# Kernel tuning notes

Measured on AMD Instinct MI355X. Metric: run time of the kernel, lower is better.

Reference implementation:

```python
import jax, jax.numpy as jnp
import numpy as np
from jax import lax

HID = 512   # hidden_dim
DI = 1024   # d_inner = ssm_ratio * hidden_dim
N = 64      # ssm_d_state
R = 32      # dt_rank = ceil(512/16)
K = 4       # k_group
B, H, W = 4, 32, 32
MLP = 2048  # mlp_ratio * hidden_dim


def _ln(x, w, b):
    m = x.mean(-1, keepdims=True)
    v = ((x - m) ** 2).mean(-1, keepdims=True)
    return (x - m) / jnp.sqrt(v + 1e-5) * w + b


def setup_inputs() -> dict:
    key = jax.random.key(0)
    ks = jax.random.split(key, 12)
    rn = lambda k, s, sc: jax.random.normal(k, s, jnp.float32) * sc
    inp = {}
    inp["content"] = rn(ks[0], (B, H, W, HID), 1.0)
    inp["style"] = rn(ks[1], (B, H, W, HID), 1.0)
    inp["norm1_w"] = jnp.ones((HID,), jnp.float32)
    inp["norm1_b"] = jnp.zeros((HID,), jnp.float32)
    inp["in_proj_w"] = rn(ks[2], (HID, 2 * DI), HID ** -0.5)
    inp["conv_w"] = rn(ks[3], (DI, 1, 3, 3), 1.0 / 3.0)  # depthwise
    inp["conv_b"] = jnp.zeros((DI,), jnp.float32)
    inp["style_proj_w"] = rn(ks[4], (HID, K * (R + N)), HID ** -0.5)
    inp["content_proj_w"] = rn(ks[5], (DI, K * N), DI ** -0.5)
    inp["dt_projs_weight"] = rn(ks[6], (K, DI, R), R ** -0.5)
    inp["dt_projs_bias"] = rn(ks[7], (K, DI), 0.1)
    inp["A_logs"] = rn(ks[8], (K * DI, N), 0.1)
    inp["Ds"] = jnp.ones((K * DI,), jnp.float32)
    inp["out_proj_w"] = rn(ks[9], (DI, HID), DI ** -0.5)
    inp["norm2_w"] = jnp.ones((HID,), jnp.float32)
    inp["norm2_b"] = jnp.zeros((HID,), jnp.float32)
    inp["mlp_w1"] = rn(ks[10], (HID, MLP), HID ** -0.5)
    inp["mlp_b1"] = jnp.zeros((MLP,), jnp.float32)
    inp["mlp_w2"] = rn(ks[11], (MLP, HID), MLP ** -0.5)
    inp["mlp_b2"] = jnp.zeros((HID,), jnp.float32)
    return inp


def reference(content, style, norm1_w, norm1_b, in_proj_w, conv_w, conv_b,
              style_proj_w, content_proj_w, dt_projs_weight, dt_projs_bias,
              A_logs, Ds, out_proj_w, norm2_w, norm2_b,
              mlp_w1, mlp_b1, mlp_w2, mlp_b2):
    Bb, Hh, Ww, C = content.shape
    L = Hh * Ww
    res1 = content
    cn = _ln(content, norm1_w, norm1_b)
    sn = _ln(style, norm1_w, norm1_b)  # norm1 shared, as in source
    xz = cn @ in_proj_w                 # (B,H,W,2*DI)
    x, z = jnp.split(xz, 2, axis=-1)
    xc = x.transpose(0, 3, 1, 2)        # (B,DI,H,W)
    xconv = lax.conv_general_dilated(
        xc, conv_w, (1, 1), 'SAME', feature_group_count=DI,
        dimension_numbers=('NCHW', 'OIHW', 'NCHW')) + conv_b[None, :, None, None]
    xa = jax.nn.silu(xconv)             # (B,DI,H,W)
    # style-derived dt/B, content-derived C
    sp = (sn @ style_proj_w).reshape(Bb, L, K * (R + N))
    dts_rank, Bs = jnp.split(sp, [K * R], axis=-1)
    Cs = (xa.transpose(0, 2, 3, 1) @ content_proj_w).reshape(Bb, L, K * N)
    # cross_scan: 4 directions (raster, transposed raster, and their flips)
    xf = xa.reshape(Bb, DI, L)
    xt = xa.transpose(0, 1, 3, 2).reshape(Bb, DI, L)
    xs = jnp.stack([xf, xt, xf[..., ::-1], xt[..., ::-1]], axis=1)  # (B,K,DI,L)
    dts_rank = dts_rank.reshape(Bb, L, K, R).transpose(0, 2, 3, 1)   # (B,K,R,L)
    dts = jnp.einsum('bkrl,kdr->bkdl', dts_rank, dt_projs_weight)    # (B,K,DI,L)
    Bsm = Bs.reshape(Bb, L, K, N).transpose(0, 2, 3, 1)              # (B,K,N,L)
    Csm = Cs.reshape(Bb, L, K, N).transpose(0, 2, 3, 1)              # (B,K,N,L)
    A = -jnp.exp(A_logs.astype(jnp.float32)).reshape(K, DI, N)
    delta = jax.nn.softplus(dts + dt_projs_bias[None, :, :, None])   # (B,K,DI,L)
    # selective scan: h_t = exp(delta_t*A)*h_{t-1} + delta_t*B_t*u_t ; y_t = <h_t, C_t>
    def step(h, inpt):
        u_t, d_t, B_t, C_t = inpt  # (B,K,DI),(B,K,DI),(B,K,N),(B,K,N)
        h = jnp.exp(d_t[..., None] * A) * h + (d_t * u_t)[..., None] * B_t[:, :, None, :]
        y = jnp.einsum('bkdn,bkn->bkd', h, C_t)
        return h, y
    h0 = jnp.zeros((Bb, K, DI, N), jnp.float32)
    seq = (xs.transpose(3, 0, 1, 2), delta.transpose(3, 0, 1, 2),
           Bsm.transpose(3, 0, 1, 2), Csm.transpose(3, 0, 1, 2))
    _, ys = lax.scan(step, h0, seq)                                  # (L,B,K,DI)
    y_scan = ys.transpose(1, 2, 3, 0) + xs * Ds.reshape(K, DI)[None, :, :, None]
    # source sums the 4 directions without un-flipping (faithful)
    y = y_scan.reshape(Bb, K, DI, Hh, Ww).sum(1).transpose(0, 2, 3, 1)  # (B,H,W,DI)
    y = (y * z) @ out_proj_w
    x1 = res1 + y
    xn = _ln(x1, norm2_w, norm2_b)
    m = jax.nn.gelu(xn @ mlp_w1 + mlp_b1, approximate=False) @ mlp_w2 + mlp_b2
    return x1 + m
```

## Files before the change

kernel.cpp:

```cpp
#include <hip/hip_runtime.h>

#define B_ 4
#define Hh_ 32
#define Ww_ 32
#define L_ 1024
#define HID_ 512
#define DI_ 1024
#define N_ 64
#define R_ 32
#define K_ 4
#define MLP_ 2048

typedef __bf16 bf16x8 __attribute__((ext_vector_type(8)));
typedef float f32x4 __attribute__((ext_vector_type(4)));
typedef float v2f __attribute__((ext_vector_type(2)));

__device__ __forceinline__ unsigned short f2bf(float f) {
  unsigned int u = __builtin_bit_cast(unsigned int, f);
  return (unsigned short)((u + 0x7FFFu + ((u >> 16) & 1u)) >> 16);
}
__device__ __forceinline__ float bf2f(unsigned short h) {
  return __builtin_bit_cast(float, (unsigned int)h << 16);
}

__device__ __forceinline__ void gload16(const unsigned short* g, unsigned short* l) {
  __builtin_amdgcn_global_load_lds(
      (const __attribute__((address_space(1))) unsigned int*)g,
      (__attribute__((address_space(3))) unsigned int*)l, 16, 0, 0);
}

template <int CTRL>
__device__ __forceinline__ float dpp_add(float x) {
  int i = __builtin_bit_cast(int, x);
  int j = __builtin_amdgcn_update_dpp(i, i, CTRL, 0xF, 0xF, false);
  return x + __builtin_bit_cast(float, j);
}

__global__ __launch_bounds__(256) void transpose_all(
    const float* __restrict__ s0, const float* __restrict__ s1,
    const float* __restrict__ s2, const float* __restrict__ s3,
    const float* __restrict__ s4, const float* __restrict__ s5,
    unsigned short* __restrict__ t0, unsigned short* __restrict__ t1,
    unsigned short* __restrict__ t2, unsigned short* __restrict__ t3,
    unsigned short* __restrict__ t4, unsigned short* __restrict__ t5) {
  __shared__ float t[32][33];
  int bid = blockIdx.x;
  const float* src; unsigned short* dst; int K, N, bx, by;
  if (bid < 1024)      { src = s0; dst = t0; K = 512;  N = 2048; int r = bid;        bx = r & 63; by = r >> 6; }
  else if (bid < 1216) { src = s1; dst = t1; K = 512;  N = 384;  int r = bid - 1024; bx = r % 12; by = r / 12; }
  else if (bid < 1472) { src = s2; dst = t2; K = 1024; N = 256;  int r = bid - 1216; bx = r & 7;  by = r >> 3; }
  else if (bid < 1984) { src = s3; dst = t3; K = 1024; N = 512;  int r = bid - 1472; bx = r & 15; by = r >> 4; }
  else if (bid < 3008) { src = s4; dst = t4; K = 512;  N = 2048; int r = bid - 1984; bx = r & 63; by = r >> 6; }
  else                 { src = s5; dst = t5; K = 2048; N = 512;  int r = bid - 3008; bx = r & 15; by = r >> 4; }
  int nb = bx * 32, kb = by * 32;
  int tx = threadIdx.x & 31, ty = threadIdx.x >> 5;
  for (int r = ty; r < 32; r += 8) t[r][tx] = src[(size_t)(kb + r) * N + nb + tx];
  __syncthreads();
  for (int r = ty; r < 32; r += 8) dst[(size_t)(nb + r) * K + kb + tx] = f2bf(t[tx][r]);
}

__global__ __launch_bounds__(256) void ln_kernel(
    const float* __restrict__ in0, unsigned short* __restrict__ out0,
    const float* __restrict__ in1, unsigned short* __restrict__ out1,
    const float* __restrict__ w, const float* __restrict__ bb) {
  const float* in = blockIdx.y ? in1 : in0;
  unsigned short* out = blockIdx.y ? out1 : out0;
  int row = blockIdx.x * 4 + (threadIdx.x >> 6);
  int lane = threadIdx.x & 63;
  const float* p = in + (size_t)row * HID_;
  float4 v0 = *(const float4*)(p + lane * 4);
  float4 v1 = *(const float4*)(p + 256 + lane * 4);
  float s = v0.x + v0.y + v0.z + v0.w + v1.x + v1.y + v1.z + v1.w;
  float q = v0.x * v0.x + v0.y * v0.y + v0.z * v0.z + v0.w * v0.w +
            v1.x * v1.x + v1.y * v1.y + v1.z * v1.z + v1.w * v1.w;
  #pragma unroll
  for (int m = 1; m < 64; m <<= 1) { s += __shfl_xor(s, m, 64); q += __shfl_xor(q, m, 64); }
  float mean = s * (1.f / 512.f);
  float var = q * (1.f / 512.f) - mean * mean;
  float rstd = rsqrtf(var + 1e-5f);
  float4 w0 = *(const float4*)(w + lane * 4);
  float4 w1 = *(const float4*)(w + 256 + lane * 4);
  float4 b0 = *(const float4*)(bb + lane * 4);
  float4 b1 = *(const float4*)(bb + 256 + lane * 4);
  unsigned short* o = out + (size_t)row * HID_;
  ushort4 r0, r1;
  r0.x = f2bf((v0.x - mean) * rstd * w0.x + b0.x);
  r0.y = f2bf((v0.y - mean) * rstd * w0.y + b0.y);
  r0.z = f2bf((v0.z - mean) * rstd * w0.z + b0.z);
  r0.w = f2bf((v0.w - mean) * rstd * w0.w + b0.w);
  r1.x = f2bf((v1.x - mean) * rstd * w1.x + b1.x);
  r1.y = f2bf((v1.y - mean) * rstd * w1.y + b1.y);
  r1.z = f2bf((v1.z - mean) * rstd * w1.z + b1.z);
  r1.w = f2bf((v1.w - mean) * rstd * w1.w + b1.w);
  *(ushort4*)(o + lane * 4) = r0;
  *(ushort4*)(o + 256 + lane * 4) = r1;
}

#define BM 128
#define BN 128
#define BK 64

template <int EPI, int OUTBF>
__global__ __launch_bounds__(256) void gemm_kernel(
    const unsigned short* __restrict__ A, const unsigned short* __restrict__ BT,
    void* __restrict__ Cv, int M, int N, int K,
    const float* __restrict__ bias, const float* __restrict__ resid) {
  __shared__ __align__(16) unsigned short As[BM * BK];
  __shared__ __align__(16) unsigned short Bs[BN * BK];
  int tid = threadIdx.x;
  int lane = tid & 63, wv = tid >> 6;
  int wm = wv >> 1, wn = wv & 1;
  int nwg = gridDim.x * gridDim.y;
  int flat = blockIdx.y * gridDim.x + blockIdx.x;
  int swz = (flat & 7) * (nwg >> 3) + (flat >> 3);
  int bx = swz % gridDim.x, by = swz / gridDim.x;
  int m0 = by * BM, n0 = bx * BN;
  f32x4 acc[4][4] = {};
  int rowblk = lane >> 3;
  int sblk = (lane & 7) ^ rowblk;
  int rA = wm * 64 + (lane & 15);
  int rB = wn * 64 + (lane & 15);
  for (int k0 = 0; k0 < K; k0 += BK) {
    __syncthreads();
    #pragma unroll
    for (int it = 0; it < 4; ++it) {
      int r0 = wv * 32 + it * 8;
      gload16(A + (size_t)(m0 + r0 + rowblk) * K + k0 + sblk * 8, &As[r0 * BK]);
      gload16(BT + (size_t)(n0 + r0 + rowblk) * K + k0 + sblk * 8, &Bs[r0 * BK]);
    }
    __syncthreads();
    #pragma unroll
    for (int kx = 0; kx < 2; ++kx) {
      int bidx = (lane >> 4) + kx * 4;
      bf16x8 fa[4], fb[4];
      #pragma unroll
      for (int i = 0; i < 4; ++i) {
        int ra = rA + i * 16;
        int rb = rB + i * 16;
        fa[i] = *(const bf16x8*)&As[ra * BK + ((bidx ^ (ra & 7)) << 3)];
        fb[i] = *(const bf16x8*)&Bs[rb * BK + ((bidx ^ (rb & 7)) << 3)];
      }
      #pragma unroll
      for (int i = 0; i < 4; ++i)
        #pragma unroll
        for (int j = 0; j < 4; ++j)
          acc[i][j] = __builtin_amdgcn_mfma_f32_16x16x32_bf16(fa[i], fb[j], acc[i][j], 0, 0, 0);
    }
  }
  int crow0 = m0 + wm * 64 + (lane >> 4) * 4, ccol0 = n0 + wn * 64 + (lane & 15);
  #pragma unroll
  for (int i = 0; i < 4; ++i) {
    #pragma unroll
    for (int j = 0; j < 4; ++j) {
      int col = ccol0 + j * 16;
      #pragma unroll
      for (int r = 0; r < 4; ++r) {
        int row = crow0 + i * 16 + r;
        float v = acc[i][j][r];
        if (EPI == 1) v += resid[(size_t)row * N + col];
        if (EPI == 2) { v += bias[col]; v = 0.5f * v * (1.f + erff(v * 0.70710678f)); }
        if (EPI == 3) v += bias[col] + resid[(size_t)row * N + col];
        if (OUTBF) ((unsigned short*)Cv)[(size_t)row * N + col] = f2bf(v);
        else       ((float*)Cv)[(size_t)row * N + col] = v;
      }
    }
  }
}

template <int EPI, int OUTBF>
__global__ __launch_bounds__(256) void gemm64_kernel(
    const unsigned short* __restrict__ A, const unsigned short* __restrict__ BT,
    void* __restrict__ Cv, int M, int N, int K,
    const float* __restrict__ bias, const float* __restrict__ resid) {
  __shared__ __align__(16) unsigned short As[64 * BK];
  __shared__ __align__(16) unsigned short Bs[128 * BK];
  int tid = threadIdx.x;
  int lane = tid & 63, wv = tid >> 6;
  int wm = wv >> 1, wn = wv & 1;
  int nwg = gridDim.x * gridDim.y;
  int flat = blockIdx.y * gridDim.x + blockIdx.x;
  int swz = (flat & 7) * (nwg >> 3) + (flat >> 3);
  int bx = swz % gridDim.x, by = swz / gridDim.x;
  int m0 = by * 64, n0 = bx * BN;
  f32x4 acc[2][4] = {};
  int rowblk = lane >> 3;
  int sblk = (lane & 7) ^ rowblk;
  int rA = wm * 32 + (lane & 15);
  int rB = wn * 64 + (lane & 15);
  for (int k0 = 0; k0 < K; k0 += BK) {
    __syncthreads();
    #pragma unroll
    for (int it = 0; it < 2; ++it) {
      int r0 = wv * 16 + it * 8;
      gload16(A + (size_t)(m0 + r0 + rowblk) * K + k0 + sblk * 8, &As[r0 * BK]);
    }
    #pragma unroll
    for (int it = 0; it < 4; ++it) {
      int r0 = wv * 32 + it * 8;
      gload16(BT + (size_t)(n0 + r0 + rowblk) * K + k0 + sblk * 8, &Bs[r0 * BK]);
    }
    __syncthreads();
    #pragma unroll
    for (int kx = 0; kx < 2; ++kx) {
      int bidx = (lane >> 4) + kx * 4;
      bf16x8 fa[2], fb[4];
      #pragma unroll
      for (int i = 0; i < 2; ++i) {
        int ra = rA + i * 16;
        fa[i] = *(const bf16x8*)&As[ra * BK + ((bidx ^ (ra & 7)) << 3)];
      }
      #pragma unroll
      for (int j = 0; j < 4; ++j) {
        int rb = rB + j * 16;
        fb[j] = *(const bf16x8*)&Bs[rb * BK + ((bidx ^ (rb & 7)) << 3)];
      }
      #pragma unroll
      for (int i = 0; i < 2; ++i)
        #pragma unroll
        for (int j = 0; j < 4; ++j)
          acc[i][j] = __builtin_amdgcn_mfma_f32_16x16x32_bf16(fa[i], fb[j], acc[i][j], 0, 0, 0);
    }
  }
  int crow0 = m0 + wm * 32 + (lane >> 4) * 4, ccol0 = n0 + wn * 64 + (lane & 15);
  #pragma unroll
  for (int i = 0; i < 2; ++i) {
    #pragma unroll
    for (int j = 0; j < 4; ++j) {
      int col = ccol0 + j * 16;
      #pragma unroll
      for (int r = 0; r < 4; ++r) {
        int row = crow0 + i * 16 + r;
        float v = acc[i][j][r];
        if (EPI == 1) v += resid[(size_t)row * N + col];
        if (EPI == 2) { v += bias[col]; v = 0.5f * v * (1.f + erff(v * 0.70710678f)); }
        if (EPI == 3) v += bias[col] + resid[(size_t)row * N + col];
        if (OUTBF) ((unsigned short*)Cv)[(size_t)row * N + col] = f2bf(v);
        else       ((float*)Cv)[(size_t)row * N + col] = v;
      }
    }
  }
}

__global__ __launch_bounds__(256) void conv_kernel(
    const unsigned short* __restrict__ xz, const float* __restrict__ cw,
    const float* __restrict__ cb, unsigned short* __restrict__ xa) {
  int idx = blockIdx.x * 256 + threadIdx.x;
  int d = idx & (DI_ - 1);
  int l = (idx >> 10) & (L_ - 1);
  int b = idx >> 20;
  int hh = l >> 5, ww = l & 31;
  float acc = cb[d];
  #pragma unroll
  for (int dh = -1; dh <= 1; ++dh) {
    int y = hh + dh;
    if ((unsigned)y >= 32u) continue;
    #pragma unroll
    for (int dw = -1; dw <= 1; ++dw) {
      int x = ww + dw;
      if ((unsigned)x >= 32u) continue;
      acc = fmaf(bf2f(xz[((size_t)b * L_ + y * 32 + x) * (2 * DI_) + d]),
                 cw[d * 9 + (dh + 1) * 3 + (dw + 1)], acc);
    }
  }
  float sv = acc / (1.f + __expf(-acc));
  xa[idx] = f2bf(sv);
}

__global__ __launch_bounds__(256) void delta_kernel(
    const float* __restrict__ sp, const float* __restrict__ dtw,
    const float* __restrict__ dtb, unsigned short* __restrict__ delta) {
  int bk = blockIdx.x;
  int b = bk >> 2, k = bk & 3;
  int dc = blockIdx.y * 256;
  int l0 = blockIdx.z * 128;
  __shared__ float wl[32 * 257];
  __shared__ float rl[128 * 32];
  int tid = threadIdx.x;
  for (int i = tid; i < 256 * 32; i += 256) {
    int dl = i >> 5, r = i & 31;
    wl[r * 257 + dl] = dtw[((size_t)k * DI_ + dc + dl) * R_ + r];
  }
  for (int i = tid; i < 128 * 32; i += 256) {
    int ll = i >> 5, r = i & 31;
    rl[ll * 32 + r] = sp[((size_t)b * L_ + l0 + ll) * 384 + k * R_ + r];
  }
  __syncthreads();
  float bias = dtb[k * DI_ + dc + tid];
  for (int ll = 0; ll < 128; ++ll) {
    float acc = bias;
    #pragma unroll
    for (int r = 0; r < 32; ++r)
      acc = fmaf(rl[ll * 32 + r], wl[r * 257 + tid], acc);
    float dlt = (acc > 15.f) ? acc : log1pf(__expf(acc));
    delta[(((size_t)(b * 4 + k) * L_) + l0 + ll) * DI_ + dc + tid] = f2bf(dlt);
  }
}

#define CH 16
#define NCH (L_ / CH)
#define DLP 36
#define YQP 6
__global__ __launch_bounds__(512) void scan_kernel(
    unsigned short* __restrict__ ybuf, const unsigned short* __restrict__ xa,
    const float* __restrict__ sp, const float* __restrict__ Cs,
    const unsigned short* __restrict__ dltb,
    const float* __restrict__ A_logs, const float* __restrict__ Ds) {
  int dblk = blockIdx.x;
  int k = blockIdx.y, b = blockIdx.z;
  int tid = threadIdx.x, lane = tid & 63, wv = tid >> 6;
  int dg = lane >> 4, ng = lane & 15;
  int qp = (lane >> 2) & 3;
  int wd = wv * 4 + dg;
  int gd = k * DI_ + dblk * 32 + wd;
  v2f a2p[2], h2[2];
  #pragma unroll
  for (int j = 0; j < 2; ++j) {
    a2p[j].x = -__expf(A_logs[(size_t)gd * N_ + ng * 4 + 2 * j]) * 1.44269504f;
    a2p[j].y = -__expf(A_logs[(size_t)gd * N_ + ng * 4 + 2 * j + 1]) * 1.44269504f;
    h2[j].x = 0.f; h2[j].y = 0.f;
  }

  __shared__ float Bsh[2][CH][64];
  __shared__ float Csh[2][CH][64];
  __shared__ float DLU[2][32][DLP];
  __shared__ float yq[CH][32][YQP];
  __shared__ float dsh[32];

  const size_t spB = (size_t)b * L_ * 384 + 128 + k * 64;
  const size_t csB = (size_t)b * L_ * 256 + k * 64;
  const size_t dlB = ((size_t)(b * 4 + k) * L_) * DI_ + dblk * 32;
  const size_t xaB = (size_t)b * L_ * DI_ + dblk * 32;

  if (tid < 32) dsh[tid] = Ds[k * DI_ + dblk * 32 + tid];

  int liS = tid >> 5, js = tid & 31;
  int liE = tid >> 5, dd = tid & 31;
  auto posf = [&](int l) {
    int lr = 1023 - l;
    return (k == 0) ? l
         : (k == 1) ? ((l & 31) * 32 + (l >> 5))
         : (k == 2) ? lr
                    : ((lr & 31) * 32 + (lr >> 5));
  };

  {
    *(float2*)&Bsh[0][liS][js * 2] = *(const float2*)(sp + spB + (size_t)liS * 384 + js * 2);
    *(float2*)&Csh[0][liS][js * 2] = *(const float2*)(Cs + csB + (size_t)liS * 256 + js * 2);
    float2 p;
    p.x = bf2f(dltb[dlB + (size_t)liS * DI_ + js]);
    p.y = bf2f(xa[xaB + (size_t)posf(liS) * DI_ + js]);
    *(float2*)&DLU[0][js][liS * 2] = p;
  }
  __syncthreads();

  int cur = 0;
  for (int c = 0; c < NCH; ++c) {
    float2 pB, pC;
    unsigned short pD, pU;
    if (c < NCH - 1) {
      int lb = (c + 1) * CH + liS;
      pB = *(const float2*)(sp + spB + (size_t)lb * 384 + js * 2);
      pC = *(const float2*)(Cs + csB + (size_t)lb * 256 + js * 2);
      pD = dltb[dlB + (size_t)lb * DI_ + js];
      pU = xa[xaB + (size_t)posf(lb) * DI_ + js];
    }
    #pragma unroll
    for (int li2 = 0; li2 < CH; li2 += 2) {
      f32x4 duq = *(const f32x4*)&DLU[cur][wd][li2 * 2];
      #pragma unroll
      for (int s = 0; s < 2; ++s) {
        int li = li2 + s;
        float dlt = s ? duq[2] : duq[0];
        float u   = s ? duq[3] : duq[1];
        float du = dlt * u;
        f32x4 bq = *(const f32x4*)&Bsh[cur][li][ng * 4];
        f32x4 cq = *(const f32x4*)&Csh[cur][li][ng * 4];
        v2f b01 = __builtin_shufflevector(bq, bq, 0, 1);
        v2f b23 = __builtin_shufflevector(bq, bq, 2, 3);
        v2f c01 = __builtin_shufflevector(cq, cq, 0, 1);
        v2f c23 = __builtin_shufflevector(cq, cq, 2, 3);
        v2f dlt2; dlt2.x = dlt; dlt2.y = dlt;
        v2f du2;  du2.x = du;  du2.y = du;
        v2f arg0 = dlt2 * a2p[0];
        v2f arg1 = dlt2 * a2p[1];
        v2f e0, e1;
        e0.x = __builtin_amdgcn_exp2f(arg0.x);
        e0.y = __builtin_amdgcn_exp2f(arg0.y);
        e1.x = __builtin_amdgcn_exp2f(arg1.x);
        e1.y = __builtin_amdgcn_exp2f(arg1.y);
        h2[0] = e0 * h2[0] + du2 * b01;
        h2[1] = e1 * h2[1] + du2 * b23;
        v2f yv = h2[0] * c01 + h2[1] * c23;
        float yp = yv.x + yv.y;
        yp = dpp_add<0xB1>(yp);
        yp = dpp_add<0x4E>(yp);
        yq[li][wd][qp] = yp;
      }
    }
    __syncthreads();
    {
      float2 q01 = *(const float2*)&yq[liE][dd][0];
      float2 q23 = *(const float2*)&yq[liE][dd][2];
      float y = (q01.x + q01.y) + (q23.x + q23.y);
      float u = DLU[cur][dd][liE * 2 + 1];
      y = fmaf(u, dsh[dd], y);
      ybuf[dlB + (size_t)(c * CH + liE) * DI_ + dd] = f2bf(y);
    }
    if (c < NCH - 1) {
      int nxt = cur ^ 1;
      *(float2*)&Bsh[nxt][liS][js * 2] = pB;
      *(float2*)&Csh[nxt][liS][js * 2] = pC;
      float2 p; p.x = bf2f(pD); p.y = bf2f(pU);
      *(float2*)&DLU[nxt][js][liS * 2] = p;
    }
    __syncthreads();
    cur ^= 1;
  }
}

__global__ __launch_bounds__(256) void fuse_ygz(
    const unsigned short* __restrict__ yk, const unsigned short* __restrict__ xz,
    unsigned short* __restrict__ ygz) {
  size_t i = ((size_t)blockIdx.x * 256 + threadIdx.x) * 8;
  size_t b = i >> 20, ld = i & ((1u << 20) - 1);
  float acc[8] = {};
  #pragma unroll
  for (int k = 0; k < 4; ++k) {
    uint4 v = *(const uint4*)(yk + ((size_t)(b * 4 + k) << 20) + ld);
    unsigned int w[4] = {v.x, v.y, v.z, v.w};
    #pragma unroll
    for (int t = 0; t < 4; ++t) {
      acc[t * 2 + 0] += __builtin_bit_cast(float, w[t] << 16);
      acc[t * 2 + 1] += __builtin_bit_cast(float, w[t] & 0xFFFF0000u);
    }
  }
  uint4 zv = *(const uint4*)(xz + (i >> 10) * (2 * DI_) + DI_ + (i & (DI_ - 1)));
  unsigned int zw[4] = {zv.x, zv.y, zv.z, zv.w};
  float z[8];
  #pragma unroll
  for (int t = 0; t < 4; ++t) {
    z[t * 2 + 0] = __builtin_bit_cast(float, zw[t] << 16);
    z[t * 2 + 1] = __builtin_bit_cast(float, zw[t] & 0xFFFF0000u);
  }
  uint4 o;
  o.x = (unsigned int)f2bf(acc[0] * z[0]) | ((unsigned int)f2bf(acc[1] * z[1]) << 16);
  o.y = (unsigned int)f2bf(acc[2] * z[2]) | ((unsigned int)f2bf(acc[3] * z[3]) << 16);
  o.z = (unsigned int)f2bf(acc[4] * z[4]) | ((unsigned int)f2bf(acc[5] * z[5]) << 16);
  o.w = (unsigned int)f2bf(acc[6] * z[6]) | ((unsigned int)f2bf(acc[7] * z[7]) << 16);
  *(uint4*)(ygz + i) = o;
}

extern "C" void kernel_launch(void* const* d_in, const int* in_sizes, int n_in,
                              void* d_out, int out_size, void* d_ws, size_t ws_size,
                              hipStream_t stream) {
  (void)in_sizes; (void)n_in; (void)out_size; (void)ws_size;
  const float* content   = (const float*)d_in[0];
  const float* style     = (const float*)d_in[1];
  const float* norm1_w   = (const float*)d_in[2];
  const float* norm1_b   = (const float*)d_in[3];
  const float* in_proj_w = (const float*)d_in[4];
  const float* conv_w    = (const float*)d_in[5];
  const float* conv_b    = (const float*)d_in[6];
  const float* style_proj_w   = (const float*)d_in[7];
  const float* content_proj_w = (const float*)d_in[8];
  const float* dtw       = (const float*)d_in[9];
  const float* dtb       = (const float*)d_in[10];
  const float* A_logs    = (const float*)d_in[11];
  const float* Ds        = (const float*)d_in[12];
  const float* out_proj_w = (const float*)d_in[13];
  const float* norm2_w   = (const float*)d_in[14];
  const float* norm2_b   = (const float*)d_in[15];
  const float* mlp_w1    = (const float*)d_in[16];
  const float* mlp_b1    = (const float*)d_in[17];
  const float* mlp_w2    = (const float*)d_in[18];
  const float* mlp_b2    = (const float*)d_in[19];
  float* out = (float*)d_out;

  float* ws = (float*)d_ws;
  const size_t ROWS = (size_t)B_ * L_;
  const size_t SCAN_ELEMS = (size_t)B_ * K_ * L_ * DI_;
  size_t o = 0;
  unsigned short* cn  = (unsigned short*)(ws + o); o += ROWS * HID_ / 2;
  unsigned short* sn  = (unsigned short*)(ws + o); o += ROWS * HID_ / 2;
  unsigned short* xn  = (unsigned short*)(ws + o); o += ROWS * HID_ / 2;
  unsigned short* xz  = (unsigned short*)(ws + o); o += ROWS * 2 * DI_ / 2;
  float* sp    = ws + o; o += ROWS * 384;
  unsigned short* xa = (unsigned short*)(ws + o); o += ROWS * DI_ / 2;
  float* csb   = ws + o; o += ROWS * 256;
  float* x1    = ws + o; o += ROWS * HID_;
  unsigned short* dltb = (unsigned short*)(ws + o); o += SCAN_ELEMS / 2;
  unsigned short* ybuf = (unsigned short*)(ws + o); o += SCAN_ELEMS / 2;
  unsigned short* ygz  = (unsigned short*)(ws + o); o += ROWS * DI_ / 2;
  unsigned short* wt = (unsigned short*)(ws + o);
  unsigned short* inpT = wt;
  unsigned short* styT = inpT + 2048 * 512;
  unsigned short* conT = styT + 384 * 512;
  unsigned short* outT = conT + 256 * 1024;
  unsigned short* w1T  = outT + 512 * 1024;
  unsigned short* w2T  = w1T + 2048 * 512;
  unsigned short* hmid = ybuf;

  transpose_all<<<4032, 256, 0, stream>>>(
      in_proj_w, style_proj_w, content_proj_w, out_proj_w, mlp_w1, mlp_w2,
      inpT, styT, conT, outT, w1T, w2T);

  ln_kernel<<<dim3(ROWS / 4, 2), 256, 0, stream>>>(content, cn, style, sn, norm1_w, norm1_b);

  gemm_kernel<0, 1><<<dim3(2048 / BN, ROWS / BM), 256, 0, stream>>>(
      cn, inpT, xz, ROWS, 2048, 512, nullptr, nullptr);
  gemm64_kernel<0, 0><<<dim3(384 / BN, ROWS / 64), 256, 0, stream>>>(
      sn, styT, sp, ROWS, 384, 512, nullptr, nullptr);
  conv_kernel<<<(ROWS * DI_) / 256, 256, 0, stream>>>(xz, conv_w, conv_b, xa);
  gemm64_kernel<0, 0><<<dim3(256 / BN, ROWS / 64), 256, 0, stream>>>(
      xa, conT, csb, ROWS, 256, 1024, nullptr, nullptr);
  delta_kernel<<<dim3(B_ * K_, DI_ / 256, L_ / 128), 256, 0, stream>>>(sp, dtw, dtb, dltb);
  scan_kernel<<<dim3(DI_ / 32, K_, B_), 512, 0, stream>>>(
      ybuf, xa, sp, csb, dltb, A_logs, Ds);
  fuse_ygz<<<(ROWS * DI_) / (256 * 8), 256, 0, stream>>>(ybuf, xz, ygz);
  gemm64_kernel<1, 0><<<dim3(512 / BN, ROWS / 64), 256, 0, stream>>>(
      ygz, outT, x1, ROWS, 512, 1024, nullptr, content);
  ln_kernel<<<dim3(ROWS / 4, 1), 256, 0, stream>>>(x1, xn, nullptr, nullptr, norm2_w, norm2_b);
  gemm_kernel<2, 1><<<dim3(2048 / BN, ROWS / BM), 256, 0, stream>>>(
      xn, w1T, hmid, ROWS, 2048, 512, mlp_b1, nullptr);
  gemm64_kernel<3, 0><<<dim3(512 / BN, ROWS / 64), 256, 0, stream>>>(
      hmid, w2T, out, ROWS, 512, 2048, mlp_b2, x1);
}
```

Baseline: 464.0 us.

## Use MFMA for dt projection, bf16 intermediates, and two channels per scan lane

Replaces the scalar-FMA delta kernel with an MFMA bf16 GEMM and softplus epilogue, using a newly cast bf16 copy of dt_projs_weight. The style and content projections now write bf16 instead of fp32, so the scan loads less data. The scan kernel gives each lane two d-channels, which halves the grid and reuses the B/C shared-memory loads across both channels. This cuts memory traffic and ALU work at the cost of lower precision for B, C and the dt inputs, and fewer scan blocks in flight.

```diff
diff --git a/kernel.cpp b/kernel.cpp
--- a/kernel.cpp
+++ b/kernel.cpp
@@ -21,6 +21,12 @@
 }
 __device__ __forceinline__ float bf2f(unsigned short h) {
   return __builtin_bit_cast(float, (unsigned int)h << 16);
+}
+__device__ __forceinline__ float2 bfp2f(unsigned int u) {
+  float2 r;
+  r.x = __builtin_bit_cast(float, u << 16);
+  r.y = __builtin_bit_cast(float, u & 0xFFFF0000u);
+  return r;
 }
 
 __device__ __forceinline__ void gload16(const unsigned short* g, unsigned short* l) {
@@ -57,6 +63,14 @@
   for (int r = ty; r < 32; r += 8) t[r][tx] = src[(size_t)(kb + r) * N + nb + tx];
   __syncthreads();
   for (int r = ty; r < 32; r += 8) dst[(size_t)(nb + r) * K + kb + tx] = f2bf(t[tx][r]);
+}
+
+__global__ __launch_bounds__(256) void cast_bf(
+    const float* __restrict__ src, unsigned short* __restrict__ dst) {
+  int i = (blockIdx.x * 256 + threadIdx.x) * 4;
+  float4 v = *(const float4*)(src + i);
+  ushort4 o = {f2bf(v.x), f2bf(v.y), f2bf(v.z), f2bf(v.w)};
+  *(ushort4*)(dst + i) = o;
 }
 
 __global__ __launch_bounds__(256) void ln_kernel(
@@ -241,6 +255,59 @@
   }
 }
 
+__global__ __launch_bounds__(256) void dtgemm_kernel(
+    const unsigned short* __restrict__ sp, const unsigned short* __restrict__ dtwB,
+    const float* __restrict__ dtb, unsigned short* __restrict__ delta) {
+  int kq = blockIdx.z;
+  int m0 = blockIdx.y * 64, n0 = blockIdx.x * 128;
+  __shared__ __align__(16) unsigned short As[64 * 32];
+  __shared__ __align__(16) unsigned short Bs[128 * 32];
+  int tid = threadIdx.x, lane = tid & 63, wv = tid >> 6;
+  int wm = wv >> 1, wn = wv & 1;
+  {
+    int r = tid >> 2, c = (tid & 3) * 8;
+    *(uint4*)&As[r * 32 + c] = *(const uint4*)(sp + (size_t)(m0 + r) * 384 + kq * 32 + c);
+  }
+  {
+    int r = tid >> 1, c = (tid & 1) * 16;
+    const unsigned short* p = dtwB + (size_t)(kq * DI_ + n0 + r) * 32 + c;
+    *(uint4*)&Bs[r * 32 + c] = *(const uint4*)(p);
+    *(uint4*)&Bs[r * 32 + c + 8] = *(const uint4*)(p + 8);
+  }
+  __syncthreads();
+  int kk = (lane >> 4) * 8;
+  int rA = wm * 32 + (lane & 15);
+  int rB = wn * 64 + (lane & 15);
+  f32x4 acc[2][4] = {};
+  bf16x8 fa[2], fb[4];
+  #pragma unroll
+  for (int i = 0; i < 2; ++i) fa[i] = *(const bf16x8*)&As[(rA + i * 16) * 32 + kk];
+  #pragma unroll
+  for (int j = 0; j < 4; ++j) fb[j] = *(const bf16x8*)&Bs[(rB + j * 16) * 32 + kk];
+  #pragma unroll
+  for (int i = 0; i < 2; ++i)
+    #pragma unroll
+    for (int j = 0; j < 4; ++j)
+      acc[i][j] = __builtin_amdgcn_mfma_f32_16x16x32_bf16(fa[i], fb[j], acc[i][j], 0, 0, 0);
+  int crow0 = m0 + wm * 32 + (lane >> 4) * 4, ccol0 = n0 + wn * 64 + (lane & 15);
+  #pragma unroll
+  for (int i = 0; i < 2; ++i) {
+    #pragma unroll
+    for (int j = 0; j < 4; ++j) {
+      int col = ccol0 + j * 16;
+      float bias = dtb[kq * DI_ + col];
+      #pragma unroll
+      for (int r = 0; r < 4; ++r) {
+        int row = crow0 + i * 16 + r;
+        float v = acc[i][j][r] + bias;
+        v = (v > 15.f) ? v : log1pf(__expf(v));
+        int bb = row >> 10, l = row & 1023;
+        delta[(((size_t)(bb * 4 + kq)) << 20) + ((size_t)l << 10) + col] = f2bf(v);
+      }
+    }
+  }
+}
+
 __global__ __launch_bounds__(256) void conv_kernel(
     const unsigned short* __restrict__ xz, const float* __restrict__ cw,
     const float* __restrict__ cb, unsigned short* __restrict__ xa) {
@@ -266,43 +333,11 @@
   xa[idx] = f2bf(sv);
 }
 
-__global__ __launch_bounds__(256) void delta_kernel(
-    const float* __restrict__ sp, const float* __restrict__ dtw,
-    const float* __restrict__ dtb, unsigned short* __restrict__ delta) {
-  int bk = blockIdx.x;
-  int b = bk >> 2, k = bk & 3;
-  int dc = blockIdx.y * 256;
-  int l0 = blockIdx.z * 128;
-  __shared__ float wl[32 * 257];
-  __shared__ float rl[128 * 32];
-  int tid = threadIdx.x;
-  for (int i = tid; i < 256 * 32; i += 256) {
-    int dl = i >> 5, r = i & 31;
-    wl[r * 257 + dl] = dtw[((size_t)k * DI_ + dc + dl) * R_ + r];
-  }
-  for (int i = tid; i < 128 * 32; i += 256) {
-    int ll = i >> 5, r = i & 31;
-    rl[ll * 32 + r] = sp[((size_t)b * L_ + l0 + ll) * 384 + k * R_ + r];
-  }
-  __syncthreads();
-  float bias = dtb[k * DI_ + dc + tid];
-  for (int ll = 0; ll < 128; ++ll) {
-    float acc = bias;
-    #pragma unroll
-    for (int r = 0; r < 32; ++r)
-      acc = fmaf(rl[ll * 32 + r], wl[r * 257 + tid], acc);
-    float dlt = (acc > 15.f) ? acc : log1pf(__expf(acc));
-    delta[(((size_t)(b * 4 + k) * L_) + l0 + ll) * DI_ + dc + tid] = f2bf(dlt);
-  }
-}
-
 #define CH 16
 #define NCH (L_ / CH)
-#define DLP 36
-#define YQP 6
 __global__ __launch_bounds__(512) void scan_kernel(
     unsigned short* __restrict__ ybuf, const unsigned short* __restrict__ xa,
-    const float* __restrict__ sp, const float* __restrict__ Cs,
+    const unsigned short* __restrict__ sp, const unsigned short* __restrict__ Cs,
     const unsigned short* __restrict__ dltb,
     const float* __restrict__ A_logs, const float* __restrict__ Ds) {
   int dblk = blockIdx.x;
@@ -310,31 +345,38 @@
   int tid = threadIdx.x, lane = tid & 63, wv = tid >> 6;
   int dg = lane >> 4, ng = lane & 15;
   int qp = (lane >> 2) & 3;
-  int wd = wv * 4 + dg;
-  int gd = k * DI_ + dblk * 32 + wd;
-  v2f a2p[2], h2[2];
-  #pragma unroll
-  for (int j = 0; j < 2; ++j) {
-    a2p[j].x = -__expf(A_logs[(size_t)gd * N_ + ng * 4 + 2 * j]) * 1.44269504f;
-    a2p[j].y = -__expf(A_logs[(size_t)gd * N_ + ng * 4 + 2 * j + 1]) * 1.44269504f;
-    h2[j].x = 0.f; h2[j].y = 0.f;
+  int wd0 = wv * 8 + dg;
+  int slot = wv * 4 + dg;
+  int gd0 = k * DI_ + dblk * 64 + wd0;
+  v2f a2p[2][2], h2[2][2];
+  {
+    f32x4 al0 = *(const f32x4*)(A_logs + (size_t)gd0 * N_ + ng * 4);
+    f32x4 al1 = *(const f32x4*)(A_logs + (size_t)(gd0 + 4) * N_ + ng * 4);
+    a2p[0][0].x = -__expf(al0[0]) * 1.44269504f; a2p[0][0].y = -__expf(al0[1]) * 1.44269504f;
+    a2p[0][1].x = -__expf(al0[2]) * 1.44269504f; a2p[0][1].y = -__expf(al0[3]) * 1.44269504f;
+    a2p[1][0].x = -__expf(al1[0]) * 1.44269504f; a2p[1][0].y = -__expf(al1[1]) * 1.44269504f;
+    a2p[1][1].x = -__expf(al1[2]) * 1.44269504f; a2p[1][1].y = -__expf(al1[3]) * 1.44269504f;
+    #pragma unroll
+    for (int di = 0; di < 2; ++di)
+      #pragma unroll
+      for (int j = 0; j < 2; ++j) { h2[di][j].x = 0.f; h2[di][j].y = 0.f; }
   }
 
   __shared__ float Bsh[2][CH][64];
   __shared__ float Csh[2][CH][64];
-  __shared__ float DLU[2][32][DLP];
-  __shared__ float yq[CH][32][YQP];
-  __shared__ float dsh[32];
+  __shared__ float DLUp[2][CH][32][4];
+  __shared__ float yq[CH][32][4][2];
+  __shared__ float dsh[64];
 
   const size_t spB = (size_t)b * L_ * 384 + 128 + k * 64;
   const size_t csB = (size_t)b * L_ * 256 + k * 64;
-  const size_t dlB = ((size_t)(b * 4 + k) * L_) * DI_ + dblk * 32;
-  const size_t xaB = (size_t)b * L_ * DI_ + dblk * 32;
-
-  if (tid < 32) dsh[tid] = Ds[k * DI_ + dblk * 32 + tid];
+  const size_t dlB = ((size_t)(b * 4 + k) * L_) * DI_ + dblk * 64;
+  const size_t xaB = (size_t)b * L_ * DI_ + dblk * 64;
+
+  if (tid < 64) dsh[tid] = Ds[k * DI_ + dblk * 64 + tid];
 
   int liS = tid >> 5, js = tid & 31;
-  int liE = tid >> 5, dd = tid & 31;
+  int d0S = (js >> 2) * 8 + (js & 3);
   auto posf = [&](int l) {
     int lr = 1023 - l;
     return (k == 0) ? l
@@ -344,74 +386,89 @@
   };
 
   {
-    *(float2*)&Bsh[0][liS][js * 2] = *(const float2*)(sp + spB + (size_t)liS * 384 + js * 2);
-    *(float2*)&Csh[0][liS][js * 2] = *(const float2*)(Cs + csB + (size_t)liS * 256 + js * 2);
-    float2 p;
-    p.x = bf2f(dltb[dlB + (size_t)liS * DI_ + js]);
-    p.y = bf2f(xa[xaB + (size_t)posf(liS) * DI_ + js]);
-    *(float2*)&DLU[0][js][liS * 2] = p;
+    float2 fB = bfp2f(*(const unsigned int*)(sp + spB + (size_t)liS * 384 + js * 2));
+    float2 fC = bfp2f(*(const unsigned int*)(Cs + csB + (size_t)liS * 256 + js * 2));
+    *(float2*)&Bsh[0][liS][js * 2] = fB;
+    *(float2*)&Csh[0][liS][js * 2] = fC;
+    int pp = posf(liS);
+    f32x4 w;
+    w[0] = bf2f(dltb[dlB + (size_t)liS * DI_ + d0S]);
+    w[1] = bf2f(xa[xaB + (size_t)pp * DI_ + d0S]);
+    w[2] = bf2f(dltb[dlB + (size_t)liS * DI_ + d0S + 4]);
+    w[3] = bf2f(xa[xaB + (size_t)pp * DI_ + d0S + 4]);
+    *(f32x4*)&DLUp[0][liS][js][0] = w;
   }
   __syncthreads();
 
   int cur = 0;
   for (int c = 0; c < NCH; ++c) {
-    float2 pB, pC;
-    unsigned short pD, pU;
+    unsigned int pB, pC;
+    unsigned short pD0, pD1, pU0, pU1;
     if (c < NCH - 1) {
       int lb = (c + 1) * CH + liS;
-      pB = *(const float2*)(sp + spB + (size_t)lb * 384 + js * 2);
-      pC = *(const float2*)(Cs + csB + (size_t)lb * 256 + js * 2);
-      pD = dltb[dlB + (size_t)lb * DI_ + js];
-      pU = xa[xaB + (size_t)posf(lb) * DI_ + js];
-    }
-    #pragma unroll
-    for (int li2 = 0; li2 < CH; li2 += 2) {
-      f32x4 duq = *(const f32x4*)&DLU[cur][wd][li2 * 2];
-      #pragma unroll
-      for (int s = 0; s < 2; ++s) {
-        int li = li2 + s;
-        float dlt = s ? duq[2] : duq[0];
-        float u   = s ? duq[3] : duq[1];
+      pB = *(const unsigned int*)(sp + spB + (size_t)lb * 384 + js * 2);
+      pC = *(const unsigned int*)(Cs + csB + (size_t)lb * 256 + js * 2);
+      pD0 = dltb[dlB + (size_t)lb * DI_ + d0S];
+      pD1 = dltb[dlB + (size_t)lb * DI_ + d0S + 4];
+      int pp = posf(lb);
+      pU0 = xa[xaB + (size_t)pp * DI_ + d0S];
+      pU1 = xa[xaB + (size_t)pp * DI_ + d0S + 4];
+    }
+    #pragma unroll
+    for (int li = 0; li < CH; ++li) {
+      f32x4 duq = *(const f32x4*)&DLUp[cur][li][slot][0];
+      f32x4 bq = *(const f32x4*)&Bsh[cur][li][ng * 4];
+      f32x4 cq = *(const f32x4*)&Csh[cur][li][ng * 4];
+      v2f b01 = __builtin_shufflevector(bq, bq, 0, 1);
+      v2f b23 = __builtin_shufflevector(bq, bq, 2, 3);
+      v2f c01 = __builtin_shufflevector(cq, cq, 0, 1);
+      v2f c23 = __builtin_shufflevector(cq, cq, 2, 3);
+      float yps0, yps1;
+      #pragma unroll
+      for (int di = 0; di < 2; ++di) {
+        float dlt = di ? duq[2] : duq[0];
+        float u   = di ? duq[3] : duq[1];
         float du = dlt * u;
-        f32x4 bq = *(const f32x4*)&Bsh[cur][li][ng * 4];
-        f32x4 cq = *(const f32x4*)&Csh[cur][li][ng * 4];
-        v2f b01 = __builtin_shufflevector(bq, bq, 0, 1);
-        v2f b23 = __builtin_shufflevector(bq, bq, 2, 3);
-        v2f c01 = __builtin_shufflevector(cq, cq, 0, 1);
-        v2f c23 = __builtin_shufflevector(cq, cq, 2, 3);
         v2f dlt2; dlt2.x = dlt; dlt2.y = dlt;
         v2f du2;  du2.x = du;  du2.y = du;
-        v2f arg0 = dlt2 * a2p[0];
-        v2f arg1 = dlt2 * a2p[1];
+        v2f arg0 = dlt2 * a2p[di][0];
+        v2f arg1 = dlt2 * a2p[di][1];
         v2f e0, e1;
         e0.x = __builtin_amdgcn_exp2f(arg0.x);
         e0.y = __builtin_amdgcn_exp2f(arg0.y);
         e1.x = __builtin_amdgcn_exp2f(arg1.x);
         e1.y = __builtin_amdgcn_exp2f(arg1.y);
-        h2[0] = e0 * h2[0] + du2 * b01;
-        h2[1] = e1 * h2[1] + du2 * b23;
-        v2f yv = h2[0] * c01 + h2[1] * c23;
+        h2[di][0] = e0 * h2[di][0] + du2 * b01;
+        h2[di][1] = e1 * h2[di][1] + du2 * b23;
+        v2f yv = h2[di][0] * c01 + h2[di][1] * c23;
         float yp = yv.x + yv.y;
         yp = dpp_add<0xB1>(yp);
         yp = dpp_add<0x4E>(yp);
-        yq[li][wd][qp] = yp;
-      }
+        if (di) yps1 = yp; else yps0 = yp;
+      }
+      float2 pr; pr.x = yps0; pr.y = yps1;
+      *(float2*)&yq[li][slot][qp][0] = pr;
     }
     __syncthreads();
     {
-      float2 q01 = *(const float2*)&yq[liE][dd][0];
-      float2 q23 = *(const float2*)&yq[liE][dd][2];
-      float y = (q01.x + q01.y) + (q23.x + q23.y);
-      float u = DLU[cur][dd][liE * 2 + 1];
-      y = fmaf(u, dsh[dd], y);
-      ybuf[dlB + (size_t)(c * CH + liE) * DI_ + dd] = f2bf(y);
+      f32x4 q0 = *(const f32x4*)&yq[liS][js][0][0];
+      f32x4 q1 = *(const f32x4*)&yq[liS][js][2][0];
+      float y0 = (q0[0] + q0[2]) + (q1[0] + q1[2]);
+      float y1 = (q0[1] + q0[3]) + (q1[1] + q1[3]);
+      f32x4 du4 = *(const f32x4*)&DLUp[cur][liS][js][0];
+      y0 = fmaf(du4[1], dsh[d0S], y0);
+      y1 = fmaf(du4[3], dsh[d0S + 4], y1);
+      size_t yb = dlB + (size_t)(c * CH + liS) * DI_;
+      ybuf[yb + d0S] = f2bf(y0);
+      ybuf[yb + d0S + 4] = f2bf(y1);
     }
     if (c < NCH - 1) {
       int nxt = cur ^ 1;
-      *(float2*)&Bsh[nxt][liS][js * 2] = pB;
-      *(float2*)&Csh[nxt][liS][js * 2] = pC;
-      float2 p; p.x = bf2f(pD); p.y = bf2f(pU);
-      *(float2*)&DLU[nxt][js][liS * 2] = p;
+      *(float2*)&Bsh[nxt][liS][js * 2] = bfp2f(pB);
+      *(float2*)&Csh[nxt][liS][js * 2] = bfp2f(pC);
+      f32x4 w;
+      w[0] = bf2f(pD0); w[1] = bf2f(pU0); w[2] = bf2f(pD1); w[3] = bf2f(pU1);
+      *(f32x4*)&DLUp[nxt][liS][js][0] = w;
     }
     __syncthreads();
     cur ^= 1;
@@ -484,9 +541,9 @@
   unsigned short* sn  = (unsigned short*)(ws + o); o += ROWS * HID_ / 2;
   unsigned short* xn  = (unsigned short*)(ws + o); o += ROWS * HID_ / 2;
   unsigned short* xz  = (unsigned short*)(ws + o); o += ROWS * 2 * DI_ / 2;
-  float* sp    = ws + o; o += ROWS * 384;
-  unsigned short* xa = (unsigned short*)(ws + o); o += ROWS * DI_ / 2;
-  float* csb   = ws + o; o += ROWS * 256;
+  unsigned short* sp  = (unsigned short*)(ws + o); o += ROWS * 384 / 2;
+  unsigned short* xa  = (unsigned short*)(ws + o); o += ROWS * DI_ / 2;
+  unsigned short* csb = (unsigned short*)(ws + o); o += ROWS * 256 / 2;
   float* x1    = ws + o; o += ROWS * HID_;
   unsigned short* dltb = (unsigned short*)(ws + o); o += SCAN_ELEMS / 2;
   unsigned short* ybuf = (unsigned short*)(ws + o); o += SCAN_ELEMS / 2;
@@ -498,23 +555,25 @@
   unsigned short* outT = conT + 256 * 1024;
   unsigned short* w1T  = outT + 512 * 1024;
   unsigned short* w2T  = w1T + 2048 * 512;
+  unsigned short* dtwB = w2T + 512 * 2048;
   unsigned short* hmid = ybuf;
 
   transpose_all<<<4032, 256, 0, stream>>>(
       in_proj_w, style_proj_w, content_proj_w, out_proj_w, mlp_w1, mlp_w2,
       inpT, styT, conT, outT, w1T, w2T);
+  cast_bf<<<(K_ * DI_ * R_) / 1024, 256, 0, stream>>>(dtw, dtwB);
 
   ln_kernel<<<dim3(ROWS / 4, 2), 256, 0, stream>>>(content, cn, style, sn, norm1_w, norm1_b);
 
   gemm_kernel<0, 1><<<dim3(2048 / BN, ROWS / BM), 256, 0, stream>>>(
       cn, inpT, xz, ROWS, 2048, 512, nullptr, nullptr);
-  gemm64_kernel<0, 0><<<dim3(384 / BN, ROWS / 64), 256, 0, stream>>>(
+  gemm64_kernel<0, 1><<<dim3(384 / BN, ROWS / 64), 256, 0, stream>>>(
       sn, styT, sp, ROWS, 384, 512, nullptr, nullptr);
   conv_kernel<<<(ROWS * DI_) / 256, 256, 0, stream>>>(xz, conv_w, conv_b, xa);
-  gemm64_kernel<0, 0><<<dim3(256 / BN, ROWS / 64), 256, 0, stream>>>(
+  gemm64_kernel<0, 1><<<dim3(256 / BN, ROWS / 64), 256, 0, stream>>>(
       xa, conT, csb, ROWS, 256, 1024, nullptr, nullptr);
-  delta_kernel<<<dim3(B_ * K_, DI_ / 256, L_ / 128), 256, 0, stream>>>(sp, dtw, dtb, dltb);
-  scan_kernel<<<dim3(DI_ / 32, K_, B_), 512, 0, stream>>>(
+  dtgemm_kernel<<<dim3(DI_ / 128, ROWS / 64, K_), 256, 0, stream>>>(sp, dtwB, dtb, dltb);
+  scan_kernel<<<dim3(DI_ / 64, K_, B_), 512, 0, stream>>>(
       ybuf, xa, sp, csb, dltb, A_logs, Ds);
   fuse_ygz<<<(ROWS * DI_) / (256 * 8), 256, 0, stream>>>(ybuf, xz, ygz);
   gemm64_kernel<1, 0><<<dim3(512 / BN, ROWS / 64), 256, 0, stream>>>(
```

New measurement: 461.2 us. No clear change (-0.6%).
